# Optimization experiments

Measured on AMD Instinct MI355X. Metric: run time of the kernel, lower is better.

Reference implementation:

```python
import jax, jax.numpy as jnp
import numpy as np

B, S, D = 2, 2048, 2048
H, DK, DV = 16, 128, 128
K_DIM = H * DK
V_DIM = H * DV
CONV_DIM = 2 * K_DIM + V_DIM
KS = 4
EPS = 1e-6


def setup_inputs() -> dict:
    key = jax.random.key(0)
    ks = jax.random.split(key, 9)
    sc = lambda k, shape, s=0.02: jax.random.normal(k, shape, jnp.float32) * s
    return {
        "hidden_states": jax.random.normal(ks[0], (B, S, D), jnp.float32),
        "attention_mask": jnp.ones((B, S), jnp.float32),
        "W_qkv": sc(ks[1], (CONV_DIM, D)),
        "conv_w": sc(ks[2], (CONV_DIM, 1, KS), 0.2),   # depthwise kernel [C,1,K]
        "conv_b": jnp.zeros((CONV_DIM,), jnp.float32),
        "W_z": sc(ks[3], (V_DIM, D)),
        "W_b": sc(ks[4], (H, D)),
        "W_a": sc(ks[5], (H, D)),
        "dt_bias": jnp.ones((H,), jnp.float32),
        "A_log": jnp.log(jax.random.uniform(ks[6], (H,), jnp.float32, 0.5, 8.0)),
        "norm_weight": jnp.zeros((DV,), jnp.float32),
        "W_out": sc(ks[7], (D, V_DIM)),
    }


def _l2norm(x):
    return x * jax.lax.rsqrt(jnp.sum(x * x, -1, keepdims=True) + 1e-6)


def _gated_delta_rule(q, k, v, g, beta):
    # q,k: [B,S,H,DK]; v: [B,S,H,DV]; g,beta: [B,S,H]
    q = _l2norm(q) * (DK ** -0.5)
    k = _l2norm(k)

    def step(state, inp):
        # state: [B,H,DK,DV]
        qt, kt, vt, gt, bt = inp
        state = state * jnp.exp(gt)[..., None, None]          # gated decay
        kv = jnp.einsum('bhk,bhkv->bhv', kt, state)           # k^T S
        delta = (vt - kv) * bt[..., None]                     # delta-rule correction
        state = state + kt[..., :, None] * delta[..., None, :]
        ot = jnp.einsum('bhk,bhkv->bhv', qt, state)
        return state, ot

    xs = tuple(jnp.moveaxis(a, 1, 0) for a in (q, k, v, g, beta))  # time-major
    state0 = jnp.zeros((B, H, DK, DV), jnp.float32)
    _, o = jax.lax.scan(step, state0, xs)
    return jnp.moveaxis(o, 0, 1)  # [B,S,H,DV]


def reference(hidden_states, attention_mask, W_qkv, conv_w, conv_b, W_z, W_b,
              W_a, dt_bias, A_log, norm_weight, W_out):
    x = hidden_states * attention_mask[:, :, None]
    mixed = jnp.einsum('bsd,cd->bsc', x, W_qkv)               # [B,S,CONV_DIM]
    # causal depthwise conv over time
    xc = jnp.moveaxis(mixed, 1, 2)                            # [B,C,S]
    xc = jax.lax.conv_general_dilated(xc, conv_w, (1,), [(KS - 1, 0)],
                                      feature_group_count=CONV_DIM)
    xc = xc + conv_b[None, :, None]
    mixed = jax.nn.silu(jnp.moveaxis(xc, 2, 1))               # [B,S,C]
    q, k, v = jnp.split(mixed, [K_DIM, 2 * K_DIM], axis=-1)
    q = q.reshape(B, S, H, DK)
    k = k.reshape(B, S, H, DK)
    v = v.reshape(B, S, H, DV)
    z = jnp.einsum('bsd,vd->bsv', x, W_z).reshape(B, S, H, DV)
    beta = jax.nn.sigmoid(jnp.einsum('bsd,hd->bsh', x, W_b))
    g = -jnp.exp(A_log) * jax.nn.softplus(jnp.einsum('bsd,hd->bsh', x, W_a) + dt_bias)
    o = _gated_delta_rule(q, k, v, g, beta)                   # [B,S,H,DV]
    # gated RMSNorm over head_v_dim
    o = o * jax.lax.rsqrt(jnp.mean(o * o, -1, keepdims=True) + EPS)
    o = o * (1.0 + norm_weight)
    o = o * jax.nn.silu(z)
    return jnp.einsum('bsv,dv->bsd', o.reshape(B, S, V_DIM), W_out)
```

## Files before the change

kernel.cpp:

```cpp
#include <hip/hip_runtime.h>
#include <hip/hip_bf16.h>
#include <math.h>

#define BB 2
#define SS 2048
#define DD 2048
#define HH 16
#define CONVC 6144
#define MM (BB*SS)

#define CH 64
#define NCH 32
#define CD_KTS 0
#define CD_TV  16384
#define CD_TP  32768
#define CD_AQ  40960
#define CD_PV  49152
#define CD_PC  49408
#define CD_STRIDE 49664

typedef __bf16 bf16_t;
typedef __bf16 bf16x8 __attribute__((ext_vector_type(8)));
typedef __bf16 bf16x4 __attribute__((ext_vector_type(4)));
typedef __bf16 bf16x2 __attribute__((ext_vector_type(2)));
typedef float  f32x4  __attribute__((ext_vector_type(4)));

#define GLOBAL_AS __attribute__((address_space(1)))
#define LDS_AS    __attribute__((address_space(3)))

#define MFMA16(a,b,c) __builtin_amdgcn_mfma_f32_16x16x32_bf16((a),(b),(c),0,0,0)

__global__ __launch_bounds__(256) void cast_all_kernel(
    const float* __restrict__ hs, const float* __restrict__ amask,
    const float* __restrict__ Wqkv, const float* __restrict__ Wz,
    const float* __restrict__ Wb, const float* __restrict__ Wa,
    const float* __restrict__ Wout,
    bf16_t* __restrict__ x_bf, bf16_t* __restrict__ wB,
    bf16_t* __restrict__ wba, bf16_t* __restrict__ woutb)
{
  const long N0 = (long)MM*DD/4;
  const long N1 = N0 + (long)CONVC*DD/4;
  const long N2 = N1 + (long)DD*DD/4;
  const long N3 = N2 + 16*DD/4;
  const long N4 = N3 + 16*DD/4;
  const long N5 = N4 + (long)DD*DD/4;
  for (long i = (long)blockIdx.x*256 + threadIdx.x; i < N5; i += (long)gridDim.x*256) {
    const float* src; bf16_t* dst; float m = 1.f;
    if (i < N0)      { long j=i;    src = hs   + j*4; dst = x_bf + j*4; m = amask[(j*4)/DD]; }
    else if (i < N1) { long j=i-N0; src = Wqkv + j*4; dst = wB + j*4; }
    else if (i < N2) { long j=i-N1; src = Wz   + j*4; dst = wB + (size_t)CONVC*DD + j*4; }
    else if (i < N3) { long j=i-N2; src = Wb   + j*4; dst = wba + j*4; }
    else if (i < N4) { long j=i-N3; src = Wa   + j*4; dst = wba + 16*DD + j*4; }
    else             { long j=i-N4; src = Wout + j*4; dst = woutb + j*4; }
    float4 v = *(const float4*)src;
    bf16x4 o4;
    o4[0]=(bf16_t)(v.x*m); o4[1]=(bf16_t)(v.y*m);
    o4[2]=(bf16_t)(v.z*m); o4[3]=(bf16_t)(v.w*m);
    *(bf16x4*)dst = o4;
  }
}

__global__ __launch_bounds__(256) void betag3_kernel(
    const bf16_t* __restrict__ xbf, const bf16_t* __restrict__ wba,
    const float* __restrict__ dtb, const float* __restrict__ Alog,
    float2* __restrict__ gb_t)
{
  __shared__ f32x4 red0[4][64];
  __shared__ f32x4 red1[4][64];
  const int t = threadIdx.x;
  const int lane = t & 63, w = t >> 6;
  const int fr = lane & 15, fq = lane >> 4;
  const long tok0 = (long)blockIdx.x*16;

  f32x4 acc0 = {0,0,0,0}, acc1 = {0,0,0,0};
  const bf16_t* ar = xbf + (tok0 + fr)*DD + fq*8;
  const bf16_t* b0 = wba + fr*DD + fq*8;
  const bf16_t* b1 = wba + (16+fr)*DD + fq*8;
  #pragma unroll 4
  for (int k2=0; k2<16; ++k2) {
    int ks = k2*4 + w;
    bf16x8 a8 = *(const bf16x8*)(ar + ks*32);
    bf16x8 p8 = *(const bf16x8*)(b0 + ks*32);
    bf16x8 q8 = *(const bf16x8*)(b1 + ks*32);
    acc0 = MFMA16(a8, p8, acc0);
    acc1 = MFMA16(a8, q8, acc1);
  }
  red0[w][lane] = acc0;
  red1[w][lane] = acc1;
  __syncthreads();
  if (w == 0) {
    f32x4 s0 = red0[0][lane], s1 = red1[0][lane];
    #pragma unroll
    for (int ww=1; ww<4; ww++) { s0 += red0[ww][lane]; s1 += red1[ww][lane]; }
    const int h = fr;
    float eA = expf(Alog[h]);
    float db = dtb[h];
    #pragma unroll
    for (int r=0;r<4;r++) {
      long tok = tok0 + fq*4 + r;
      int b = (int)(tok >> 11), s = (int)(tok & (SS-1));
      float beta = 1.f/(1.f+expf(-s0[r]));
      float tt2 = s1[r] + db;
      float sp = (tt2 > 20.f) ? tt2 : log1pf(expf(tt2));
      float g  = -eA * sp;
      gb_t[((long)b*HH + h)*SS + s] = make_float2(g, beta);
    }
  }
}

__global__ __launch_bounds__(512) void gemm_fused(
    const bf16_t* __restrict__ A, const bf16_t* __restrict__ Bm,
    bf16_t* __restrict__ Cmix, bf16_t* __restrict__ Cz, int K, int nbn)
{
  extern __shared__ char gsm[];
  const int t    = threadIdx.x;
  const int lane = t & 63;
  const int wid  = t >> 6;
  const int wm   = wid >> 2, wn = wid & 3;
  const int fr   = lane & 15, fq = lane >> 4;

  const int nwg = gridDim.x;
  const int wg  = ((int)blockIdx.x & 7)*(nwg >> 3) + ((int)blockIdx.x >> 3);
  const int grp = wg / (nbn*4);
  const int rem = wg - grp*(nbn*4);
  const long bm = grp*4 + (rem & 3);
  const long bn = rem >> 2;

  int rowS[2], colS[2];
  #pragma unroll
  for (int i=0;i<2;i++) {
    int L  = (i*512 + t)*16;
    int Ls = L ^ (((L>>9)&1)<<5);
    rowS[i] = (Ls>>10)*16 + ((Ls&1023)>>6);
    colS[i] = (Ls&63)>>1;
  }
  const bf16_t* Ab = A  + (bm*256)*(long)K;
  const bf16_t* Bb = Bm + (bn*256)*(long)K;

  f32x4 acc[8][4];
  #pragma unroll
  for (int i=0;i<8;i++)
    #pragma unroll
    for (int j=0;j<4;j++) acc[i][j] = (f32x4){0.f,0.f,0.f,0.f};

  const int aoff = fr*64 + ((fq*16) ^ ((fr&8)<<2));

  auto stage = [&](int buf, int oper, int kh, int kt) {
    const bf16_t* srcb = oper ? Bb : Ab;
    char* dst0 = gsm + oper*65536 + buf*32768 + kh*16384 + t*16;
    #pragma unroll
    for (int i=0;i<2;i++) {
      const bf16_t* src = srcb + (long)rowS[i]*K + kt*64 + kh*32 + colS[i];
      __builtin_amdgcn_global_load_lds((const GLOBAL_AS void*)src,
          (LDS_AS void*)(dst0 + i*8192), 16, 0, 0);
    }
  };

  stage(0,0,0,0); stage(0,1,0,0); stage(0,0,1,0); stage(0,1,1,0);
  asm volatile("s_waitcnt vmcnt(4)" ::: "memory");
  __builtin_amdgcn_s_barrier();

  bf16x8 bfr[4];
  int cb = 0;
  const int KT = K >> 6;
  for (int kt=0; kt<KT; ++kt) {
    const int ktn = (kt+1 < KT) ? kt+1 : kt;
    const char* abuf = gsm + cb*32768;
    const char* bbuf = gsm + 65536 + cb*32768;

    #pragma unroll
    for (int ph=0; ph<4; ph++) {
      const int kh = ph >> 1, mh = ph & 1;
      bf16x8 af[4];
      #pragma unroll
      for (int j=0;j<4;j++)
        af[j] = *(const bf16x8*)(abuf + kh*16384 + (wm*8 + mh*4 + j)*1024 + aoff);
      if (mh == 0) {
        #pragma unroll
        for (int n=0;n<4;n++)
          bfr[n] = *(const bf16x8*)(bbuf + kh*16384 + (wn*4+n)*1024 + aoff);
      }
      stage(cb^1, mh, kh, ktn);
      if (mh == 1) {
        __builtin_amdgcn_sched_barrier(0);
        asm volatile("s_waitcnt vmcnt(4)" ::: "memory");
      }
      __builtin_amdgcn_sched_barrier(0);
      __builtin_amdgcn_s_barrier();
      asm volatile("s_waitcnt lgkmcnt(0)" ::: "memory");
      __builtin_amdgcn_sched_barrier(0);
      __builtin_amdgcn_s_setprio(1);
      #pragma unroll
      for (int j=0;j<4;j++)
        #pragma unroll
        for (int n=0;n<4;n++)
          acc[mh*4+j][n] = MFMA16(af[j], bfr[n], acc[mh*4+j][n]);
      __builtin_amdgcn_s_setprio(0);
    }
    cb ^= 1;
  }
  __syncthreads();

  bf16_t* Co;
  long No, colb;
  if (bn < 24) { Co = Cmix; No = CONVC; colb = bn*256; }
  else         { Co = Cz;   No = DD;    colb = (bn-24)*256; }

  #pragma unroll
  for (int mi=0;mi<8;mi++) {
    #pragma unroll
    for (int ni=0;ni<4;ni++) {
      long row = bm*256 + wm*128 + mi*16 + fq*4;
      long col = colb + wn*64 + ni*16 + fr;
      #pragma unroll
      for (int r=0;r<4;r++)
        Co[(row+r)*No + col] = (bf16_t)acc[mi][ni][r];
    }
  }
}

template<bool OUT_BF16>
__global__ __launch_bounds__(512) void gemm256(
    const bf16_t* __restrict__ A, const bf16_t* __restrict__ Bm,
    void* __restrict__ Cp, int M, int N, int K, int nbn)
{
  extern __shared__ char gsm[];
  const int t    = threadIdx.x;
  const int lane = t & 63;
  const int wid  = t >> 6;
  const int wm   = wid >> 2, wn = wid & 3;
  const int fr   = lane & 15, fq = lane >> 4;

  const int nwg = gridDim.x;
  const int wg  = ((int)blockIdx.x & 7)*(nwg >> 3) + ((int)blockIdx.x >> 3);
  const int grp = wg / (nbn*4);
  const int rem = wg - grp*(nbn*4);
  const long bm = grp*4 + (rem & 3);
  const long bn = rem >> 2;

  int rowS[2], colS[2];
  #pragma unroll
  for (int i=0;i<2;i++) {
    int L  = (i*512 + t)*16;
    int Ls = L ^ (((L>>9)&1)<<5);
    rowS[i] = (Ls>>10)*16 + ((Ls&1023)>>6);
    colS[i] = (Ls&63)>>1;
  }
  const bf16_t* Ab = A  + (bm*256)*(long)K;
  const bf16_t* Bb = Bm + (bn*128)*(long)K;

  f32x4 acc[8][2];
  #pragma unroll
  for (int i=0;i<8;i++) { acc[i][0] = (f32x4){0,0,0,0}; acc[i][1] = (f32x4){0,0,0,0}; }

  const int aoff = fr*64 + ((fq*16) ^ ((fr&8)<<2));

  auto stageA = [&](int buf, int kh, int kt) {
    char* dst0 = gsm + buf*32768 + kh*16384 + t*16;
    #pragma unroll
    for (int i=0;i<2;i++) {
      const bf16_t* src = Ab + (long)rowS[i]*K + kt*64 + kh*32 + colS[i];
      __builtin_amdgcn_global_load_lds((const GLOBAL_AS void*)src,
          (LDS_AS void*)(dst0 + i*8192), 16, 0, 0);
    }
  };
  auto stageB = [&](int buf, int kh, int kt) {
    char* dst = gsm + 65536 + buf*16384 + kh*8192 + t*16;
    const bf16_t* src = Bb + (long)rowS[0]*K + kt*64 + kh*32 + colS[0];
    __builtin_amdgcn_global_load_lds((const GLOBAL_AS void*)src,
        (LDS_AS void*)dst, 16, 0, 0);
  };

  stageA(0,0,0); stageB(0,0,0); stageA(0,1,0); stageB(0,1,0);
  asm volatile("s_waitcnt vmcnt(3)" ::: "memory");
  __builtin_amdgcn_s_barrier();

  int cb = 0;
  const int KT = K >> 6;
  for (int kt=0; kt<KT; ++kt) {
    const int ktn = (kt+1 < KT) ? kt+1 : kt;
    const char* abuf = gsm + cb*32768;
    const char* bbuf = gsm + 65536 + cb*16384;

    #pragma unroll
    for (int kh=0; kh<2; kh++) {
      bf16x8 af[8], bfr[2];
      #pragma unroll
      for (int j=0;j<8;j++)
        af[j] = *(const bf16x8*)(abuf + kh*16384 + (wm*8+j)*1024 + aoff);
      #pragma unroll
      for (int n=0;n<2;n++)
        bfr[n] = *(const bf16x8*)(bbuf + kh*8192 + (wn*2+n)*1024 + aoff);
      stageA(cb^1, kh, ktn);
      stageB(cb^1, kh, ktn);
      asm volatile("s_waitcnt vmcnt(3)" ::: "memory");
      __builtin_amdgcn_sched_barrier(0);
      __builtin_amdgcn_s_barrier();
      asm volatile("s_waitcnt lgkmcnt(0)" ::: "memory");
      __builtin_amdgcn_sched_barrier(0);
      __builtin_amdgcn_s_setprio(1);
      #pragma unroll
      for (int j=0;j<8;j++)
        #pragma unroll
        for (int n=0;n<2;n++)
          acc[j][n] = MFMA16(af[j], bfr[n], acc[j][n]);
      __builtin_amdgcn_s_setprio(0);
    }
    cb ^= 1;
  }
  __syncthreads();

  #pragma unroll
  for (int mi=0;mi<8;mi++) {
    #pragma unroll
    for (int ni=0;ni<2;ni++) {
      long row = bm*256 + wm*128 + mi*16 + fq*4;
      long col = bn*128 + wn*32 + ni*16 + fr;
      #pragma unroll
      for (int r=0;r<4;r++) {
        float v = acc[mi][ni][r];
        if (OUT_BF16) ((bf16_t*)Cp)[(row+r)*(long)N + col] = (bf16_t)v;
        else          ((float*)Cp)[(row+r)*(long)N + col] = v;
      }
    }
  }
}

__global__ __launch_bounds__(256) void conv_norm_kernel(
    const bf16_t* __restrict__ mixed, const float* __restrict__ cw,
    const float* __restrict__ cb, bf16_t* __restrict__ q_t,
    bf16_t* __restrict__ k_t, bf16_t* __restrict__ v_t)
{
  __shared__ bf16_t lx[35*392];
  __shared__ float4 lcw[384];
  __shared__ float  lcb[384];
  const int blk = blockIdx.x;
  const int st = blk & 63;
  const int h  = (blk >> 6) & 15;
  const int b  = blk >> 10;
  const int t  = threadIdx.x;
  const int s0 = st*32;

  for (int i = t; i < 384; i += 256) {
    int seg = i >> 7, d = i & 127;
    int gch = seg*2048 + h*128 + d;
    lcw[i] = ((const float4*)cw)[gch];
    lcb[i] = cb[gch];
  }
  for (int idx = t; idx < 1680; idx += 256) {
    int chunk = idx >> 4, e = idx & 15;
    int row = chunk / 3, seg = chunk - row*3;
    int s2 = s0 - 3 + row;
    bf16x8 v8;
    if (s2 >= 0) {
      v8 = *(const bf16x8*)(mixed + ((long)b*SS + s2)*CONVC + seg*2048 + h*128 + e*8);
    } else {
      #pragma unroll
      for (int j=0;j<8;j++) v8[j] = (bf16_t)0.f;
    }
    *(bf16x8*)&lx[row*392 + seg*128 + e*8] = v8;
  }
  __syncthreads();

  const int s_local = t >> 3, dg = t & 7;
  const int s  = s0 + s_local;
  const int d0 = dg*16;
  const long obase = ((long)(b*HH + h)*SS + s)*128 + d0;

  float scl_q = 0.f, scl_k = 0.f;

  #pragma unroll
  for (int seg=0; seg<3; ++seg) {
    bf16x8 xr[4][2];
    #pragma unroll
    for (int tp=0; tp<4; ++tp) {
      const bf16_t* p = &lx[(s_local + tp)*392 + seg*128 + d0];
      xr[tp][0] = *(const bf16x8*)p;
      xr[tp][1] = *(const bf16x8*)(p + 8);
    }
    float a[16];
    #pragma unroll
    for (int half=0; half<2; ++half) {
      #pragma unroll
      for (int j=0;j<8;j++) {
        int ch = seg*128 + d0 + half*8 + j;
        float4 wj = lcw[ch];
        float v = lcb[ch]
                + (float)xr[0][half][j]*wj.x + (float)xr[1][half][j]*wj.y
                + (float)xr[2][half][j]*wj.z + (float)xr[3][half][j]*wj.w;
        a[half*8+j] = v * (1.f/(1.f+expf(-v)));
      }
    }
    if (seg < 2) {
      float ss = 0.f;
      #pragma unroll
      for (int j=0;j<16;j++) ss += a[j]*a[j];
      ss += __shfl_xor(ss, 1);
      ss += __shfl_xor(ss, 2);
      ss += __shfl_xor(ss, 4);
      float scl = rsqrtf(ss + 1e-6f);
      if (seg == 0) scl_q = scl * 0.08838834764831845f;
      else          scl_k = scl;
    }
    {
      bf16_t* outp = (seg==0) ? (q_t + obase) : (seg==1) ? (k_t + obase) : (v_t + obase);
      float scl = (seg==0) ? scl_q : (seg==1) ? scl_k : 1.f;
      bf16x8 o0, o1;
      #pragma unroll
      for (int j=0;j<8;j++) { o0[j] = (bf16_t)(a[j]*scl); o1[j] = (bf16_t)(a[8+j]*scl); }
      *(bf16x8*)outp = o0;
      *(bf16x8*)(outp + 8) = o1;
    }
  }
}

__global__ __launch_bounds__(256) void chunkA_kernel(
    const bf16_t* __restrict__ q_t, const bf16_t* __restrict__ k_t,
    const bf16_t* __restrict__ v_t, const float2* __restrict__ gb_t,
    char* __restrict__ cdata)
{
  extern __shared__ char smem[];
  bf16_t* lK  = (bf16_t*)(smem);
  bf16_t* lQV = (bf16_t*)(smem + 17408);
  float*  lLf = (float*)(smem + 35840);
  float*  lXf = (float*)(smem + 52480);
  float*  gcv = (float*)(smem + 69120);
  float*  pvv = (float*)(smem + 69376);
  float*  bvv = (float*)(smem + 69632);
  float*  evv = (float*)(smem + 69888);
  float*  lP  = (float*)(smem + 70144);

  const int cd = blockIdx.x;
  const int bh = cd >> 5, c = cd & 31;
  const int t = threadIdx.x;
  const int lane = t & 63, w = t >> 6;
  const int fr = lane & 15, fq = lane >> 4;

  const bf16_t* kg = k_t + ((long)bh*SS + c*CH)*128;
  const bf16_t* qg = q_t + ((long)bh*SS + c*CH)*128;
  const bf16_t* vg = v_t + ((long)bh*SS + c*CH)*128;
  char* cdp = cdata + (long)cd*CD_STRIDE;

  #pragma unroll
  for (int ib=0; ib<4; ib++) {
    int e0 = (t + 256*ib)*8;
    int r = e0 >> 7, cc = e0 & 127;
    *(bf16x8*)&lK[r*136+cc]  = *(const bf16x8*)(kg + e0);
    *(bf16x8*)&lQV[r*136+cc] = *(const bf16x8*)(qg + e0);
  }
  if (t < 64) {
    float2 gb = gb_t[(long)bh*SS + c*CH + t];
    gcv[t] = gb.x;
    bvv[t] = gb.y;
  }
  __syncthreads();
  if (t < 64) {
    float g = gcv[t];
    #pragma unroll
    for (int off=1; off<64; off<<=1) {
      float n = __shfl_up(g, off);
      if (lane >= off) g += n;
    }
    gcv[t] = g;
  }
  __syncthreads();
  if (t < 64) {
    pvv[t] = expf(gcv[t]);
    evv[t] = expf(gcv[63] - gcv[t]);
  }

  {
    f32x4 accG[4], accQ[4];
    #pragma unroll
    for (int tn=0;tn<4;tn++){ accG[tn]=(f32x4){0,0,0,0}; accQ[tn]=(f32x4){0,0,0,0}; }
    #pragma unroll
    for (int ks=0;ks<4;ks++) {
      bf16x8 aK = *(const bf16x8*)&lK[(w*16+fr)*136 + fq*8 + ks*32];
      bf16x8 aQ = *(const bf16x8*)&lQV[(w*16+fr)*136 + fq*8 + ks*32];
      #pragma unroll
      for (int tn=0;tn<4;tn++) {
        bf16x8 bK = *(const bf16x8*)&lK[(tn*16+fr)*136 + fq*8 + ks*32];
        accG[tn] = MFMA16(aK, bK, accG[tn]);
        accQ[tn] = MFMA16(aQ, bK, accQ[tn]);
      }
    }
    bf16_t* aqg = (bf16_t*)(cdp + CD_AQ);
    #pragma unroll
    for (int tn=0;tn<4;tn++) {
      #pragma unroll
      for (int r=0;r<4;r++) {
        int tt = w*16 + fq*4 + r;
        int ii = tn*16 + fr;
        float er = expf(gcv[tt] - gcv[ii]);
        lLf[tt*65 + ii] = (ii < tt) ? bvv[tt]*er*accG[tn][r] : 0.f;
        aqg[tt*64 + ii] = (bf16_t)((ii <= tt) ? er*accQ[tn][r] : 0.f);
      }
    }
  }

  {
    const int a = w;
    float* Ub = lXf + (a*16)*65 + a*16;
    const float* Lb = lLf + (a*16)*65 + a*16;
    if (lane < 16) Ub[lane] = (lane == 0) ? 1.f : 0.f;
    for (int bb = a+1; bb < 4; bb++)
      for (int e = lane; e < 256; e += 64)
        lXf[(a*16 + (e>>4))*65 + bb*16 + (e&15)] = 0.f;
    if (lane < 16) {
      const int cc = lane;
      for (int i=1; i<16; i++) {
        float s = 0.f;
        for (int j=0; j<i; j++) s += Lb[i*65+j] * Ub[j*65+cc];
        Ub[i*65+cc] = ((i==cc)?1.f:0.f) - s;
      }
    }
  }
  __syncthreads();

  bf16_t* lVT = lQV;
  {
    const int m = t & 15;
    #pragma unroll
    for (int ib=0; ib<4; ib++) {
      int e0 = (t + 256*ib)*8;
      int r = e0 >> 7, cc = e0 & 127;
      bf16x8 v8 = *(const bf16x8*)(vg + e0);
      #pragma unroll
      for (int e=0;e<8;e++) {
        int ee = (e + m) & 7;
        lVT[(cc+ee)*72 + r] = v8[ee];
      }
    }
  }

  {
    const int i = t >> 4, j = t & 15;
    #pragma unroll
    for (int bb=0; bb<3; bb++) {
      float s = 0.f;
      const float* Mrow = lLf + ((bb+1)*16 + i)*65 + bb*16;
      const float* Ucol = lXf + (bb*16)*65 + bb*16 + j;
      #pragma unroll
      for (int k=0;k<16;k++) s += Mrow[k] * Ucol[k*65];
      lP[bb*272 + i*17 + j] = s;
    }
  }
  __syncthreads();
  {
    const int i = t >> 4, j = t & 15;
    #pragma unroll
    for (int bb=0; bb<3; bb++) {
      float s = 0.f;
      const float* Urow = lXf + ((bb+1)*16 + i)*65 + (bb+1)*16;
      const float* Pcol = lP + bb*272 + j;
      #pragma unroll
      for (int k=0;k<16;k++) s += Urow[k] * Pcol[k*17];
      lXf[((bb+1)*16 + i)*65 + bb*16 + j] = -s;
    }
  }
  __syncthreads();
  {
    const int i = t >> 4, j = t & 15;
    #pragma unroll
    for (int bb=0; bb<2; bb++) {
      float s = 0.f;
      const float* M0 = lLf + ((bb+2)*16 + i)*65 + bb*16;
      const float* U0 = lXf + (bb*16)*65 + bb*16 + j;
      const float* M1 = lLf + ((bb+2)*16 + i)*65 + (bb+1)*16;
      const float* T1 = lXf + ((bb+1)*16)*65 + bb*16 + j;
      #pragma unroll
      for (int k=0;k<16;k++) s += M0[k]*U0[k*65] + M1[k]*T1[k*65];
      lP[bb*272 + i*17 + j] = s;
    }
  }
  __syncthreads();
  {
    const int i = t >> 4, j = t & 15;
    #pragma unroll
    for (int bb=0; bb<2; bb++) {
      float s = 0.f;
      const float* Urow = lXf + ((bb+2)*16 + i)*65 + (bb+2)*16;
      const float* Pcol = lP + bb*272 + j;
      #pragma unroll
      for (int k=0;k<16;k++) s += Urow[k] * Pcol[k*17];
      lXf[((bb+2)*16 + i)*65 + bb*16 + j] = -s;
    }
  }
  __syncthreads();
  {
    const int i = t >> 4, j = t & 15;
    float s = 0.f;
    const float* M0 = lLf + (48 + i)*65 + 0;
    const float* U0 = lXf + 0*65 + j;
    const float* M1 = lLf + (48 + i)*65 + 16;
    const float* T1 = lXf + 16*65 + j;
    const float* M2 = lLf + (48 + i)*65 + 32;
    const float* T2 = lXf + 32*65 + j;
    #pragma unroll
    for (int k=0;k<16;k++) s += M0[k]*U0[k*65] + M1[k]*T1[k*65] + M2[k]*T2[k*65];
    lP[i*17 + j] = s;
  }
  __syncthreads();
  {
    const int i = t >> 4, j = t & 15;
    float s = 0.f;
    const float* Urow = lXf + (48 + i)*65 + 48;
    const float* Pcol = lP + j;
    #pragma unroll
    for (int k=0;k<16;k++) s += Urow[k] * Pcol[k*17];
    lXf[(48 + i)*65 + j] = -s;
  }
  __syncthreads();

  bf16_t* lXb = (bf16_t*)lLf;
  {
    bf16_t* tpg = (bf16_t*)(cdp + CD_TP);
    #pragma unroll
    for (int ib=0; ib<16; ib++) {
      int idx = t + ib*256; int r = idx>>6, cc = idx&63;
      float xv = lXf[r*65+cc] * bvv[cc];
      tpg[r*64+cc] = (bf16_t)(xv * pvv[cc]);
      lXb[r*72+cc] = (bf16_t)xv;
    }
  }
  __syncthreads();

  {
    f32x4 acc[8];
    #pragma unroll
    for (int tn=0;tn<8;tn++) acc[tn]=(f32x4){0,0,0,0};
    #pragma unroll
    for (int ks=0;ks<2;ks++) {
      bf16x8 aX = *(const bf16x8*)&lXb[(w*16+fr)*72 + fq*8 + ks*32];
      #pragma unroll
      for (int tn=0;tn<8;tn++) {
        bf16x8 bV = *(const bf16x8*)&lVT[(tn*16+fr)*72 + fq*8 + ks*32];
        acc[tn] = MFMA16(aX, bV, acc[tn]);
      }
    }
    bf16_t* tvg = (bf16_t*)(cdp + CD_TV);
    #pragma unroll
    for (int tn=0;tn<8;tn++)
      #pragma unroll
      for (int r=0;r<4;r++) {
        int tt = w*16 + fq*4 + r, dv = tn*16 + fr;
        tvg[tt*128 + dv] = (bf16_t)acc[tn][r];
      }
  }

  {
    bf16_t* ktg = (bf16_t*)(cdp + CD_KTS);
    int dk = t >> 1, c0 = (t & 1)*32;
    bf16_t tmp[32];
    #pragma unroll
    for (int i2=0;i2<32;i2++) {
      int i = c0 + i2;
      tmp[i2] = (bf16_t)((float)lK[i*136 + dk] * evv[i]);
    }
    #pragma unroll
    for (int s8=0;s8<4;s8++)
      *(bf16x8*)&ktg[dk*64 + c0 + s8*8] = *(bf16x8*)&tmp[s8*8];
  }
  if (t < 64) ((float*)(cdp + CD_PV))[t] = pvv[t];
  if (t == 0) *((float*)(cdp + CD_PC)) = expf(gcv[63]);
}

__global__ __launch_bounds__(256) void chunkS_kernel(
    const bf16_t* __restrict__ q_t, const bf16_t* __restrict__ k_t,
    const char* __restrict__ cdata, bf16_t* __restrict__ obuf)
{
  extern __shared__ char smem[];
  float*  lS  = (float*)(smem);
  bf16_t* lSb = (bf16_t*)(smem + 8320);
  bf16_t* lXT = (bf16_t*)(smem + 137600);
  bf16_t* lDT = (bf16_t*)(smem + 140416);

  const int bid = blockIdx.x;
  const int lb  = (bid & 7)*32 + (bid >> 3);
  const int bh = lb >> 3, sp = lb & 7;
  const int dv0 = sp*16;
  const int b = bh >> 4, h = bh & 15;
  const int t = threadIdx.x, lane = t & 63, w = t >> 6;
  const int fr = lane & 15, fq = lane >> 4;

  #pragma unroll
  for (int ib=0; ib<8; ib++) {
    int idx = t + ib*256; int r = idx>>7, cc = idx&127;
    lS[r*129+cc] = 0.f;
    lSb[r*136+cc] = (bf16_t)0.f;
  }

  const bf16_t* kg = k_t + (long)bh*SS*128;
  const bf16_t* qg = q_t + (long)bh*SS*128;

  bf16x8 kr0,kr1,kr2,kr3, qr0,qr1,qr2,qr3, kt0,kt1,kt2,kt3, tp0,tp1;

#define STAGE_LOAD(CSRC)                                                       \
  {                                                                            \
    const char* cdl = cdata + (long)(bh*NCH + (CSRC))*CD_STRIDE;               \
    const bf16_t* kl = kg + (long)(CSRC)*CH*128;                               \
    const bf16_t* ql = qg + (long)(CSRC)*CH*128;                               \
    const bf16_t* ktl = (const bf16_t*)(cdl + CD_KTS);                         \
    const bf16_t* tpl = (const bf16_t*)(cdl + CD_TP);                          \
    int e0 = t*8, e1 = (t+256)*8, e2 = (t+512)*8, e3 = (t+768)*8;              \
    kr0 = *(const bf16x8*)(kl + e0); kr1 = *(const bf16x8*)(kl + e1);          \
    kr2 = *(const bf16x8*)(kl + e2); kr3 = *(const bf16x8*)(kl + e3);          \
    qr0 = *(const bf16x8*)(ql + e0); qr1 = *(const bf16x8*)(ql + e1);          \
    qr2 = *(const bf16x8*)(ql + e2); qr3 = *(const bf16x8*)(ql + e3);          \
    kt0 = *(const bf16x8*)(ktl + e0); kt1 = *(const bf16x8*)(ktl + e1);        \
    kt2 = *(const bf16x8*)(ktl + e2); kt3 = *(const bf16x8*)(ktl + e3);        \
    tp0 = *(const bf16x8*)(tpl + e0); tp1 = *(const bf16x8*)(tpl + e1);        \
  }

#define STAGE_WRITE(BASE)                                                      \
  {                                                                            \
    char* _bp = (BASE);                                                        \
    bf16_t* _lK  = (bf16_t*)_bp;                                               \
    bf16_t* _lQ  = (bf16_t*)(_bp + 17408);                                     \
    bf16_t* _lTp = (bf16_t*)(_bp + 34816);                                     \
    bf16_t* _lKT = (bf16_t*)(_bp + 44032);                                     \
    int e0 = t*8, e1 = (t+256)*8, e2 = (t+512)*8, e3 = (t+768)*8;              \
    *(bf16x8*)&_lK[(e0>>7)*136 + (e0&127)] = kr0;                              \
    *(bf16x8*)&_lK[(e1>>7)*136 + (e1&127)] = kr1;                              \
    *(bf16x8*)&_lK[(e2>>7)*136 + (e2&127)] = kr2;                              \
    *(bf16x8*)&_lK[(e3>>7)*136 + (e3&127)] = kr3;                              \
    *(bf16x8*)&_lQ[(e0>>7)*136 + (e0&127)] = qr0;                              \
    *(bf16x8*)&_lQ[(e1>>7)*136 + (e1&127)] = qr1;                              \
    *(bf16x8*)&_lQ[(e2>>7)*136 + (e2&127)] = qr2;                              \
    *(bf16x8*)&_lQ[(e3>>7)*136 + (e3&127)] = qr3;                              \
    *(bf16x8*)&_lKT[(e0>>6)*72 + (e0&63)] = kt0;                               \
    *(bf16x8*)&_lKT[(e1>>6)*72 + (e1&63)] = kt1;                               \
    *(bf16x8*)&_lKT[(e2>>6)*72 + (e2&63)] = kt2;                               \
    *(bf16x8*)&_lKT[(e3>>6)*72 + (e3&63)] = kt3;                               \
    *(bf16x8*)&_lTp[(e0>>6)*72 + (e0&63)] = tp0;                               \
    *(bf16x8*)&_lTp[(e1>>6)*72 + (e1&63)] = tp1;                               \
  }

  STAGE_LOAD(0);
  STAGE_WRITE(smem + 12672);
  __syncthreads();

  for (int c=0; c<NCH; c++) {
    const int cd = bh*NCH + c;
    const char* cdp = cdata + (long)cd*CD_STRIDE;
    const int cb = c & 1;
    char* rbuf = smem + 12672 + cb*62464;
    bf16_t* lK  = (bf16_t*)rbuf;
    bf16_t* lQ  = (bf16_t*)(rbuf + 17408);
    bf16_t* lTp = (bf16_t*)(rbuf + 34816);
    bf16_t* lKT = (bf16_t*)(rbuf + 44032);

    float tvq0, tvq1, tvq2, tvq3, pc;
    float pvq[4];
    bf16x8 aqr0, aqr1;
    {
      const bf16_t* tvp = (const bf16_t*)(cdp + CD_TV);
      const float* pvp = (const float*)(cdp + CD_PV);
      const bf16_t* aqp = (const bf16_t*)(cdp + CD_AQ);
      tvq0 = (float)tvp[(w*16+fq*4+0)*128 + dv0 + fr];
      tvq1 = (float)tvp[(w*16+fq*4+1)*128 + dv0 + fr];
      tvq2 = (float)tvp[(w*16+fq*4+2)*128 + dv0 + fr];
      tvq3 = (float)tvp[(w*16+fq*4+3)*128 + dv0 + fr];
      #pragma unroll
      for (int r=0;r<4;r++) pvq[r] = pvp[w*16+fq*4+r];
      pc = *(const float*)(cdp + CD_PC);
      aqr0 = *(const bf16x8*)(aqp + (w*16+fr)*64 + fq*8);
      aqr1 = *(const bf16x8*)(aqp + (w*16+fr)*64 + fq*8 + 32);
    }
    const int cn = (c+1 < NCH) ? c+1 : c;
    STAGE_LOAD(cn);

    f32x4 aX = {0,0,0,0}, aXq = {0,0,0,0};
    #pragma unroll
    for (int ks=0; ks<4; ks++) {
      bf16x8 bS = *(const bf16x8*)&lSb[fr*136 + fq*8 + ks*32];
      bf16x8 aK = *(const bf16x8*)&lK[(w*16+fr)*136 + fq*8 + ks*32];
      bf16x8 aQ = *(const bf16x8*)&lQ[(w*16+fr)*136 + fq*8 + ks*32];
      aX  = MFMA16(aK, bS, aX);
      aXq = MFMA16(aQ, bS, aXq);
    }
    #pragma unroll
    for (int r=0;r<4;r++)
      lXT[fr*88 + (w*16+fq*4+r)] = (bf16_t)aX[r];
    __syncthreads();

    {
      f32x4 aD = {0,0,0,0};
      #pragma unroll
      for (int ks=0; ks<2; ks++) {
        bf16x8 aT = *(const bf16x8*)&lTp[(w*16+fr)*72 + fq*8 + ks*32];
        bf16x8 bX = *(const bf16x8*)&lXT[fr*88 + fq*8 + ks*32];
        aD = MFMA16(aT, bX, aD);
      }
      lDT[fr*88 + (w*16+fq*4+0)] = (bf16_t)(tvq0 - aD[0]);
      lDT[fr*88 + (w*16+fq*4+1)] = (bf16_t)(tvq1 - aD[1]);
      lDT[fr*88 + (w*16+fq*4+2)] = (bf16_t)(tvq2 - aD[2]);
      lDT[fr*88 + (w*16+fq*4+3)] = (bf16_t)(tvq3 - aD[3]);
    }
    __syncthreads();

    STAGE_WRITE(smem + 12672 + (cb^1)*62464);

    {
      f32x4 aS0 = {0,0,0,0}, aS1 = {0,0,0,0}, aO = {0,0,0,0};
      #pragma unroll
      for (int ks=0; ks<2; ks++) {
        bf16x8 aDd = *(const bf16x8*)&lDT[fr*88 + fq*8 + ks*32];
        bf16x8 bK0 = *(const bf16x8*)&lKT[(w*32+fr)*72 + fq*8 + ks*32];
        bf16x8 bK1 = *(const bf16x8*)&lKT[(w*32+16+fr)*72 + fq*8 + ks*32];
        bf16x8 aA  = (ks==0) ? aqr0 : aqr1;
        bf16x8 bD  = *(const bf16x8*)&lDT[fr*88 + fq*8 + ks*32];
        aS0 = MFMA16(aDd, bK0, aS0);
        aS1 = MFMA16(aDd, bK1, aS1);
        aO  = MFMA16(aA,  bD,  aO);
      }
      #pragma unroll
      for (int r=0;r<4;r++) {
        int dvr = fq*4 + r;
        float s0 = lS[dvr*129 + w*32 + fr]      * pc + aS0[r];
        float s1 = lS[dvr*129 + w*32 + 16 + fr] * pc + aS1[r];
        lS[dvr*129 + w*32 + fr]      = s0;
        lS[dvr*129 + w*32 + 16 + fr] = s1;
        lSb[dvr*136 + w*32 + fr]      = (bf16_t)s0;
        lSb[dvr*136 + w*32 + 16 + fr] = (bf16_t)s1;
      }
      #pragma unroll
      for (int r=0;r<4;r++) {
        int tt = w*16+fq*4+r;
        long tok = (long)b*SS + c*CH + tt;
        float ov = pvq[r]*aXq[r] + aO[r];
        obuf[(tok*HH + h)*128 + dv0 + fr] = (bf16_t)ov;
      }
    }
    __syncthreads();
  }
#undef STAGE_LOAD
#undef STAGE_WRITE
}

__global__ __launch_bounds__(256) void norm_gate_kernel(
    const bf16_t* __restrict__ o, const bf16_t* __restrict__ zfull,
    const float* __restrict__ nw, bf16_t* __restrict__ og)
{
  const long row = (long)blockIdx.x*4 + (threadIdx.x >> 6);
  const int lane = threadIdx.x & 63;
  const long tok = row >> 4;
  const int h = row & 15;
  bf16x2 xv = *(const bf16x2*)(o + row*128 + lane*2);
  float x0 = (float)xv[0], x1 = (float)xv[1];
  float ss = x0*x0 + x1*x1;
  #pragma unroll
  for (int off=32; off>=1; off>>=1) ss += __shfl_xor(ss, off);
  float rr = rsqrtf(ss*(1.f/128.f) + 1e-6f);
  bf16x2 zv = *(const bf16x2*)(zfull + tok*DD + h*128 + lane*2);
  float z0 = (float)zv[0], z1 = (float)zv[1];
  float v0 = x0 * rr * (1.f + nw[lane*2])   * (z0 * (1.f/(1.f+expf(-z0))));
  float v1 = x1 * rr * (1.f + nw[lane*2+1]) * (z1 * (1.f/(1.f+expf(-z1))));
  bf16x2 ov; ov[0] = (bf16_t)v0; ov[1] = (bf16_t)v1;
  *(bf16x2*)(og + row*128 + lane*2) = ov;
}

extern "C" void kernel_launch(void* const* d_in, const int* in_sizes, int n_in,
                              void* d_out, int out_size, void* d_ws, size_t ws_size,
                              hipStream_t stream)
{
  const float* hs    = (const float*)d_in[0];
  const float* amask = (const float*)d_in[1];
  const float* Wqkv  = (const float*)d_in[2];
  const float* convw = (const float*)d_in[3];
  const float* convb = (const float*)d_in[4];
  const float* Wz    = (const float*)d_in[5];
  const float* Wb    = (const float*)d_in[6];
  const float* Wa    = (const float*)d_in[7];
  const float* dtb   = (const float*)d_in[8];
  const float* Alog  = (const float*)d_in[9];
  const float* nw    = (const float*)d_in[10];
  const float* Wout  = (const float*)d_in[11];

  const size_t MB = 1024*1024;
  char* p = (char*)d_ws;
  auto alloc = [&](size_t bytes) { char* r = p; p += (bytes + 255) & ~(size_t)255; return r; };
  bf16_t* x_bf   = (bf16_t*)alloc(16*MB);
  char*   bigreg = alloc(84*MB);
  bf16_t* wba    = (bf16_t*)alloc(256*1024);
  bf16_t* woutb  = (bf16_t*)alloc(8*MB);
  bf16_t* zbuf   = (bf16_t*)alloc(16*MB);
  bf16_t* q_t    = (bf16_t*)alloc(16*MB);
  bf16_t* k_t    = (bf16_t*)alloc(16*MB);
  bf16_t* v_t    = (bf16_t*)alloc(16*MB);
  float2* gb_t   = (float2*)alloc((size_t)BB*HH*SS*8);
  size_t need = (size_t)(p - (char*)d_ws);
  if (ws_size < need) return;

  bf16_t* wB      = (bf16_t*)bigreg;
  bf16_t* mixed   = (bf16_t*)(bigreg + 34*MB);
  char*   cdata   = bigreg;
  bf16_t* obuf    = v_t;
  bf16_t* og      = q_t;

  cast_all_kernel<<<2048, 256, 0, stream>>>(hs, amask, Wqkv, Wz, Wb, Wa, Wout,
                                            x_bf, wB, wba, woutb);

  betag3_kernel<<<MM/16, 256, 0, stream>>>(x_bf, wba, dtb, Alog, gb_t);

  gemm_fused<<<512, 512, 131072, stream>>>(x_bf, wB, mixed, zbuf, DD, 32);

  conv_norm_kernel<<<BB*HH*(SS/32), 256, 0, stream>>>(mixed, convw, convb, q_t, k_t, v_t);

  chunkA_kernel<<<BB*HH*NCH, 256, 73408, stream>>>(q_t, k_t, v_t, gb_t, cdata);
  chunkS_kernel<<<BB*HH*8, 256, 143232, stream>>>(q_t, k_t, cdata, obuf);

  norm_gate_kernel<<<MM*HH/4, 256, 0, stream>>>(obuf, zbuf, nw, og);

  gemm256<false><<<256, 512, 98304, stream>>>(og, woutb, d_out, MM, DD, DD, 16);
}
```

Measured before the change: 360.2 us.

## Deepen recurrent-scan prefetch to two chunks ahead with lightweight LDS barriers

```diff
diff --git a/kernel.cpp b/kernel.cpp
--- a/kernel.cpp
+++ b/kernel.cpp
@@ -29,6 +29,11 @@
 #define LDS_AS    __attribute__((address_space(3)))
 
 #define MFMA16(a,b,c) __builtin_amdgcn_mfma_f32_16x16x32_bf16((a),(b),(c),0,0,0)
+
+#define BARX() do {                                                            \
+  asm volatile("s_waitcnt lgkmcnt(0)" ::: "memory");                           \
+  __builtin_amdgcn_s_barrier();                                                \
+} while (0)
 
 __global__ __launch_bounds__(256) void cast_all_kernel(
     const float* __restrict__ hs, const float* __restrict__ amask,
@@ -693,26 +698,58 @@
   const bf16_t* kg = k_t + (long)bh*SS*128;
   const bf16_t* qg = q_t + (long)bh*SS*128;
 
-  bf16x8 kr0,kr1,kr2,kr3, qr0,qr1,qr2,qr3, kt0,kt1,kt2,kt3, tp0,tp1;
-
-#define STAGE_LOAD(CSRC)                                                       \
+  bf16x8 kr0A,kr1A,kr2A,kr3A, qr0A,qr1A,qr2A,qr3A, kt0A,kt1A,kt2A,kt3A, tp0A,tp1A, aq0A,aq1A;
+  bf16_t tv0A,tv1A,tv2A,tv3A; float4 pvA; float pcA;
+  bf16x8 kr0B,kr1B,kr2B,kr3B, qr0B,qr1B,qr2B,qr3B, kt0B,kt1B,kt2B,kt3B, tp0B,tp1B, aq0B,aq1B;
+  bf16_t tv0B,tv1B,tv2B,tv3B; float4 pvB; float pcB;
+  float ctv0, ctv1, ctv2, ctv3, cpc; float4 cpv; bf16x8 caq0, caq1;
+
+#define LOADSET(S, CSRC)                                                       \
   {                                                                            \
-    const char* cdl = cdata + (long)(bh*NCH + (CSRC))*CD_STRIDE;               \
-    const bf16_t* kl = kg + (long)(CSRC)*CH*128;                               \
-    const bf16_t* ql = qg + (long)(CSRC)*CH*128;                               \
+    const int _c = (CSRC);                                                     \
+    const char* cdl = cdata + (long)(bh*NCH + _c)*CD_STRIDE;                   \
+    const bf16_t* kl = kg + (long)_c*CH*128;                                   \
+    const bf16_t* ql = qg + (long)_c*CH*128;                                   \
     const bf16_t* ktl = (const bf16_t*)(cdl + CD_KTS);                         \
     const bf16_t* tpl = (const bf16_t*)(cdl + CD_TP);                          \
+    const bf16_t* aql = (const bf16_t*)(cdl + CD_AQ);                          \
+    const bf16_t* tvl = (const bf16_t*)(cdl + CD_TV);                          \
     int e0 = t*8, e1 = (t+256)*8, e2 = (t+512)*8, e3 = (t+768)*8;              \
-    kr0 = *(const bf16x8*)(kl + e0); kr1 = *(const bf16x8*)(kl + e1);          \
-    kr2 = *(const bf16x8*)(kl + e2); kr3 = *(const bf16x8*)(kl + e3);          \
-    qr0 = *(const bf16x8*)(ql + e0); qr1 = *(const bf16x8*)(ql + e1);          \
-    qr2 = *(const bf16x8*)(ql + e2); qr3 = *(const bf16x8*)(ql + e3);          \
-    kt0 = *(const bf16x8*)(ktl + e0); kt1 = *(const bf16x8*)(ktl + e1);        \
-    kt2 = *(const bf16x8*)(ktl + e2); kt3 = *(const bf16x8*)(ktl + e3);        \
-    tp0 = *(const bf16x8*)(tpl + e0); tp1 = *(const bf16x8*)(tpl + e1);        \
-  }
-
-#define STAGE_WRITE(BASE)                                                      \
+    kr0##S = *(const bf16x8*)(kl + e0); kr1##S = *(const bf16x8*)(kl + e1);    \
+    kr2##S = *(const bf16x8*)(kl + e2); kr3##S = *(const bf16x8*)(kl + e3);    \
+    qr0##S = *(const bf16x8*)(ql + e0); qr1##S = *(const bf16x8*)(ql + e1);    \
+    qr2##S = *(const bf16x8*)(ql + e2); qr3##S = *(const bf16x8*)(ql + e3);    \
+    kt0##S = *(const bf16x8*)(ktl + e0); kt1##S = *(const bf16x8*)(ktl + e1);  \
+    kt2##S = *(const bf16x8*)(ktl + e2); kt3##S = *(const bf16x8*)(ktl + e3);  \
+    tp0##S = *(const bf16x8*)(tpl + e0); tp1##S = *(const bf16x8*)(tpl + e1);  \
+    aq0##S = *(const bf16x8*)(aql + (w*16+fr)*64 + fq*8);                      \
+    aq1##S = *(const bf16x8*)(aql + (w*16+fr)*64 + fq*8 + 32);                 \
+    tv0##S = tvl[(w*16+fq*4+0)*128 + dv0 + fr];                                \
+    tv1##S = tvl[(w*16+fq*4+1)*128 + dv0 + fr];                                \
+    tv2##S = tvl[(w*16+fq*4+2)*128 + dv0 + fr];                                \
+    tv3##S = tvl[(w*16+fq*4+3)*128 + dv0 + fr];                                \
+    pv##S = *(const float4*)((const float*)(cdl + CD_PV) + w*16 + fq*4);       \
+    pc##S = *(const float*)(cdl + CD_PC);                                      \
+  }
+
+#define CPD(S)                                                                 \
+  {                                                                            \
+    ctv0 = (float)tv0##S; ctv1 = (float)tv1##S;                                \
+    ctv2 = (float)tv2##S; ctv3 = (float)tv3##S;                                \
+    cpv = pv##S; cpc = pc##S; caq0 = aq0##S; caq1 = aq1##S;                    \
+  }
+
+#define CPS()                                                                  \
+  {                                                                            \
+    kr0A=kr0B; kr1A=kr1B; kr2A=kr2B; kr3A=kr3B;                                \
+    qr0A=qr0B; qr1A=qr1B; qr2A=qr2B; qr3A=qr3B;                                \
+    kt0A=kt0B; kt1A=kt1B; kt2A=kt2B; kt3A=kt3B;                                \
+    tp0A=tp0B; tp1A=tp1B; aq0A=aq0B; aq1A=aq1B;                                \
+    tv0A=tv0B; tv1A=tv1B; tv2A=tv2B; tv3A=tv3B;                                \
+    pvA=pvB; pcA=pcB;                                                          \
+  }
+
+#define STG(S, BASE)                                                           \
   {                                                                            \
     char* _bp = (BASE);                                                        \
     bf16_t* _lK  = (bf16_t*)_bp;                                               \
@@ -720,29 +757,30 @@
     bf16_t* _lTp = (bf16_t*)(_bp + 34816);                                     \
     bf16_t* _lKT = (bf16_t*)(_bp + 44032);                                     \
     int e0 = t*8, e1 = (t+256)*8, e2 = (t+512)*8, e3 = (t+768)*8;              \
-    *(bf16x8*)&_lK[(e0>>7)*136 + (e0&127)] = kr0;                              \
-    *(bf16x8*)&_lK[(e1>>7)*136 + (e1&127)] = kr1;                              \
-    *(bf16x8*)&_lK[(e2>>7)*136 + (e2&127)] = kr2;                              \
-    *(bf16x8*)&_lK[(e3>>7)*136 + (e3&127)] = kr3;                              \
-    *(bf16x8*)&_lQ[(e0>>7)*136 + (e0&127)] = qr0;                              \
-    *(bf16x8*)&_lQ[(e1>>7)*136 + (e1&127)] = qr1;                              \
-    *(bf16x8*)&_lQ[(e2>>7)*136 + (e2&127)] = qr2;                              \
-    *(bf16x8*)&_lQ[(e3>>7)*136 + (e3&127)] = qr3;                              \
-    *(bf16x8*)&_lKT[(e0>>6)*72 + (e0&63)] = kt0;                               \
-    *(bf16x8*)&_lKT[(e1>>6)*72 + (e1&63)] = kt1;                               \
-    *(bf16x8*)&_lKT[(e2>>6)*72 + (e2&63)] = kt2;                               \
-    *(bf16x8*)&_lKT[(e3>>6)*72 + (e3&63)] = kt3;                               \
-    *(bf16x8*)&_lTp[(e0>>6)*72 + (e0&63)] = tp0;                               \
-    *(bf16x8*)&_lTp[(e1>>6)*72 + (e1&63)] = tp1;                               \
-  }
-
-  STAGE_LOAD(0);
-  STAGE_WRITE(smem + 12672);
-  __syncthreads();
-
+    *(bf16x8*)&_lK[(e0>>7)*136 + (e0&127)] = kr0##S;                           \
+    *(bf16x8*)&_lK[(e1>>7)*136 + (e1&127)] = kr1##S;                           \
+    *(bf16x8*)&_lK[(e2>>7)*136 + (e2&127)] = kr2##S;                           \
+    *(bf16x8*)&_lK[(e3>>7)*136 + (e3&127)] = kr3##S;                           \
+    *(bf16x8*)&_lQ[(e0>>7)*136 + (e0&127)] = qr0##S;                           \
+    *(bf16x8*)&_lQ[(e1>>7)*136 + (e1&127)] = qr1##S;                           \
+    *(bf16x8*)&_lQ[(e2>>7)*136 + (e2&127)] = qr2##S;                           \
+    *(bf16x8*)&_lQ[(e3>>7)*136 + (e3&127)] = qr3##S;                           \
+    *(bf16x8*)&_lKT[(e0>>6)*72 + (e0&63)] = kt0##S;                            \
+    *(bf16x8*)&_lKT[(e1>>6)*72 + (e1&63)] = kt1##S;                            \
+    *(bf16x8*)&_lKT[(e2>>6)*72 + (e2&63)] = kt2##S;                            \
+    *(bf16x8*)&_lKT[(e3>>6)*72 + (e3&63)] = kt3##S;                            \
+    *(bf16x8*)&_lTp[(e0>>6)*72 + (e0&63)] = tp0##S;                            \
+    *(bf16x8*)&_lTp[(e1>>6)*72 + (e1&63)] = tp1##S;                            \
+  }
+
+  LOADSET(A, 0);
+  STG(A, smem + 12672);
+  CPD(A);
+  LOADSET(A, 1);
+  __syncthreads();
+
+  #pragma unroll 2
   for (int c=0; c<NCH; c++) {
-    const int cd = bh*NCH + c;
-    const char* cdp = cdata + (long)cd*CD_STRIDE;
     const int cb = c & 1;
     char* rbuf = smem + 12672 + cb*62464;
     bf16_t* lK  = (bf16_t*)rbuf;
@@ -750,25 +788,7 @@
     bf16_t* lTp = (bf16_t*)(rbuf + 34816);
     bf16_t* lKT = (bf16_t*)(rbuf + 44032);
 
-    float tvq0, tvq1, tvq2, tvq3, pc;
-    float pvq[4];
-    bf16x8 aqr0, aqr1;
-    {
-      const bf16_t* tvp = (const bf16_t*)(cdp + CD_TV);
-      const float* pvp = (const float*)(cdp + CD_PV);
-      const bf16_t* aqp = (const bf16_t*)(cdp + CD_AQ);
-      tvq0 = (float)tvp[(w*16+fq*4+0)*128 + dv0 + fr];
-      tvq1 = (float)tvp[(w*16+fq*4+1)*128 + dv0 + fr];
-      tvq2 = (float)tvp[(w*16+fq*4+2)*128 + dv0 + fr];
-      tvq3 = (float)tvp[(w*16+fq*4+3)*128 + dv0 + fr];
-      #pragma unroll
-      for (int r=0;r<4;r++) pvq[r] = pvp[w*16+fq*4+r];
-      pc = *(const float*)(cdp + CD_PC);
-      aqr0 = *(const bf16x8*)(aqp + (w*16+fr)*64 + fq*8);
-      aqr1 = *(const bf16x8*)(aqp + (w*16+fr)*64 + fq*8 + 32);
-    }
-    const int cn = (c+1 < NCH) ? c+1 : c;
-    STAGE_LOAD(cn);
+    LOADSET(B, (c+2 < NCH) ? c+2 : NCH-1);
 
     f32x4 aX = {0,0,0,0}, aXq = {0,0,0,0};
     #pragma unroll
@@ -782,7 +802,7 @@
     #pragma unroll
     for (int r=0;r<4;r++)
       lXT[fr*88 + (w*16+fq*4+r)] = (bf16_t)aX[r];
-    __syncthreads();
+    BARX();
 
     {
       f32x4 aD = {0,0,0,0};
@@ -792,14 +812,14 @@
         bf16x8 bX = *(const bf16x8*)&lXT[fr*88 + fq*8 + ks*32];
         aD = MFMA16(aT, bX, aD);
       }
-      lDT[fr*88 + (w*16+fq*4+0)] = (bf16_t)(tvq0 - aD[0]);
-      lDT[fr*88 + (w*16+fq*4+1)] = (bf16_t)(tvq1 - aD[1]);
-      lDT[fr*88 + (w*16+fq*4+2)] = (bf16_t)(tvq2 - aD[2]);
-      lDT[fr*88 + (w*16+fq*4+3)] = (bf16_t)(tvq3 - aD[3]);
-    }
-    __syncthreads();
-
-    STAGE_WRITE(smem + 12672 + (cb^1)*62464);
+      lDT[fr*88 + (w*16+fq*4+0)] = (bf16_t)(ctv0 - aD[0]);
+      lDT[fr*88 + (w*16+fq*4+1)] = (bf16_t)(ctv1 - aD[1]);
+      lDT[fr*88 + (w*16+fq*4+2)] = (bf16_t)(ctv2 - aD[2]);
+      lDT[fr*88 + (w*16+fq*4+3)] = (bf16_t)(ctv3 - aD[3]);
+    }
+    BARX();
+
+    STG(A, smem + 12672 + (cb^1)*62464);
 
     {
       f32x4 aS0 = {0,0,0,0}, aS1 = {0,0,0,0}, aO = {0,0,0,0};
@@ -808,34 +828,39 @@
         bf16x8 aDd = *(const bf16x8*)&lDT[fr*88 + fq*8 + ks*32];
         bf16x8 bK0 = *(const bf16x8*)&lKT[(w*32+fr)*72 + fq*8 + ks*32];
         bf16x8 bK1 = *(const bf16x8*)&lKT[(w*32+16+fr)*72 + fq*8 + ks*32];
-        bf16x8 aA  = (ks==0) ? aqr0 : aqr1;
-        bf16x8 bD  = *(const bf16x8*)&lDT[fr*88 + fq*8 + ks*32];
+        bf16x8 aA  = (ks==0) ? caq0 : caq1;
         aS0 = MFMA16(aDd, bK0, aS0);
         aS1 = MFMA16(aDd, bK1, aS1);
-        aO  = MFMA16(aA,  bD,  aO);
+        aO  = MFMA16(aA,  aDd, aO);
       }
       #pragma unroll
       for (int r=0;r<4;r++) {
         int dvr = fq*4 + r;
-        float s0 = lS[dvr*129 + w*32 + fr]      * pc + aS0[r];
-        float s1 = lS[dvr*129 + w*32 + 16 + fr] * pc + aS1[r];
+        float s0 = lS[dvr*129 + w*32 + fr]      * cpc + aS0[r];
+        float s1 = lS[dvr*129 + w*32 + 16 + fr] * cpc + aS1[r];
         lS[dvr*129 + w*32 + fr]      = s0;
         lS[dvr*129 + w*32 + 16 + fr] = s1;
         lSb[dvr*136 + w*32 + fr]      = (bf16_t)s0;
         lSb[dvr*136 + w*32 + 16 + fr] = (bf16_t)s1;
       }
+      float cpvv[4] = {cpv.x, cpv.y, cpv.z, cpv.w};
       #pragma unroll
       for (int r=0;r<4;r++) {
         int tt = w*16+fq*4+r;
         long tok = (long)b*SS + c*CH + tt;
-        float ov = pvq[r]*aXq[r] + aO[r];
+        float ov = cpvv[r]*aXq[r] + aO[r];
         obuf[(tok*HH + h)*128 + dv0 + fr] = (bf16_t)ov;
       }
     }
-    __syncthreads();
-  }
-#undef STAGE_LOAD
-#undef STAGE_WRITE
+    BARX();
+
+    CPD(A);
+    CPS();
+  }
+#undef LOADSET
+#undef CPD
+#undef CPS
+#undef STG
 }
 
 __global__ __launch_bounds__(256) void norm_gate_kernel(
```

Result: no change. 365.7 us (+1.5%).
